# Performance work log

Hardware: AMD Instinct MI355X
Metric: run time of the kernel (lower is better)

Reference implementation:

```python
import jax, jax.numpy as jnp
import numpy as np

B, T, C, H = 8, 2048, 1024, 128  # batch, seq, n_embed, head_size


def setup_inputs() -> dict:
    key = jax.random.key(0)
    ks = jax.random.split(key, 7)
    s = 1.0 / np.sqrt(C)
    return {
        "x": jax.random.normal(ks[0], (B, T, C), dtype=jnp.float32),
        "Wq": jax.random.uniform(ks[1], (C, H), jnp.float32, -s, s),
        "bq": jax.random.uniform(ks[2], (H,), jnp.float32, -s, s),
        "Wk": jax.random.uniform(ks[3], (C, H), jnp.float32, -s, s),
        "bk": jax.random.uniform(ks[4], (H,), jnp.float32, -s, s),
        "Wv": jax.random.uniform(ks[5], (C, H), jnp.float32, -s, s),
        "bv": jax.random.uniform(ks[6], (H,), jnp.float32, -s, s),
    }


def reference(x, Wq, bq, Wk, bk, Wv, bv):
    # Projections: [B, T, H]
    Q = jnp.einsum("btc,ch->bth", x, Wq) + bq
    K = jnp.einsum("btc,ch->bth", x, Wk) + bk
    V = jnp.einsum("btc,ch->bth", x, Wv) + bv
    # Scores scaled by n_embed**-0.5 (faithful to source, which uses C not head_size)
    scale = jnp.asarray(C, x.dtype) ** -0.5
    scores = jnp.einsum("bqh,bkh->bqk", Q, K) * scale  # [B, T, T]
    causal = jnp.tril(jnp.ones((T, T), dtype=bool))
    scores = jnp.where(causal, scores, jnp.asarray(-jnp.inf, x.dtype))
    attn = jax.nn.softmax(scores, axis=-1)
    # dropout p=0.0 (eval) -> identity
    return jnp.einsum("bqk,bkh->bqh", attn, V)
```

## Files before the change

### kernel.cpp

```cpp
#include <hip/hip_runtime.h>
#include <hip/hip_bf16.h>
#include <math.h>

typedef __attribute__((ext_vector_type(4))) float f32x4;
typedef __attribute__((ext_vector_type(8))) short s16x8;
typedef __attribute__((ext_vector_type(4))) short s16x4;

#define NB 8
#define NT 2048
#define NC 1024
#define NH 128
#define QSCALE 0.04508422002778f
#define PIECES 80

__device__ __forceinline__ short f2bf(float f) {
  __hip_bfloat16 h = __float2bfloat16(f);
  union { __hip_bfloat16 h; short s; } u; u.h = h;
  return u.s;
}

__device__ __forceinline__ void glds16(const short* g, short* l) {
  __builtin_amdgcn_global_load_lds(
      (const __attribute__((address_space(1))) unsigned int*)g,
      (__attribute__((address_space(3))) unsigned int*)l, 16, 0, 0);
}

__global__ __launch_bounds__(256)
void wt_kernel(const float* __restrict__ Wq, const float* __restrict__ Wk,
               const float* __restrict__ Wv, short* __restrict__ Wt) {
  __shared__ short T[64 * 72];
  const int tid = threadIdx.x;
  const int k0 = blockIdx.x * 64, n0 = blockIdx.y * 64, proj = blockIdx.z;
  const float* W = (proj == 0) ? Wq : ((proj == 1) ? Wk : Wv);
#pragma unroll
  for (int u = 0; u < 4; u++) {
    int row = u * 16 + (tid >> 4);
    int col4 = (tid & 15) * 4;
    float4 v = *(const float4*)(W + (size_t)(k0 + row) * NH + n0 + col4);
    T[(col4 + 0) * 72 + row] = f2bf(v.x);
    T[(col4 + 1) * 72 + row] = f2bf(v.y);
    T[(col4 + 2) * 72 + row] = f2bf(v.z);
    T[(col4 + 3) * 72 + row] = f2bf(v.w);
  }
  __syncthreads();
#pragma unroll
  for (int u = 0; u < 2; u++) {
    int c = tid + 256 * u;
    int n = c >> 3, c8 = c & 7;
    s16x8 v = *(const s16x8*)(T + n * 72 + c8 * 8);
    *(s16x8*)(Wt + (size_t)proj * (NH * NC) + (size_t)(n0 + n) * NC + k0 + c8 * 8) = v;
  }
}

__global__ __launch_bounds__(256, 3)
void proj_kernel(const float* __restrict__ x, const short* __restrict__ Wt,
                 const float* __restrict__ bq, const float* __restrict__ bk,
                 const float* __restrict__ bv,
                 short* __restrict__ Qb, short* __restrict__ Kb, short* __restrict__ Vtb) {
  __shared__ __align__(16) short smem[2 * 12288];

  const int tid = threadIdx.x;
  const int w = tid >> 6, lane = tid & 63;
  const int lr = lane & 15, lg = lane >> 4;
  const int proj = blockIdx.x;
  const int m0 = blockIdx.y * 64;
  const int msub = (w & 1) * 32, nsub = (w >> 1) * 64;

  const short* Wtp = Wt + (size_t)proj * (NH * NC);
  const int arow = tid >> 2, aq = tid & 3;
  const float* asrc = x + (size_t)(m0 + arow) * NC + aq * 16;

  f32x4 acc[2][4];
#pragma unroll
  for (int i = 0; i < 2; i++)
#pragma unroll
    for (int j = 0; j < 4; j++) acc[i][j] = {0.f, 0.f, 0.f, 0.f};

  float4 pa[2][4];

  auto loadA = [&](int slot, int k0) {
#pragma unroll
    for (int u = 0; u < 4; u++) pa[slot][u] = *(const float4*)(asrc + k0 + u * 4);
  };
  auto writeA = [&](int slot, int buf) {
    short* As = smem + buf * 12288;
#pragma unroll
    for (int h = 0; h < 2; h++) {
      float4 a = pa[slot][2 * h], b2 = pa[slot][2 * h + 1];
      s16x8 v;
      v[0] = f2bf(a.x); v[1] = f2bf(a.y); v[2] = f2bf(a.z); v[3] = f2bf(a.w);
      v[4] = f2bf(b2.x); v[5] = f2bf(b2.y); v[6] = f2bf(b2.z); v[7] = f2bf(b2.w);
      int cc = aq * 2 + h;
      *(s16x8*)(As + arow * 64 + ((cc ^ (arow & 7)) * 8)) = v;
    }
  };
  auto stageB = [&](int buf, int k0) {
    short* Bs = smem + buf * 12288 + 4096;
#pragma unroll
    for (int u = 0; u < 4; u++) {
      int c = u * 256 + w * 64 + lane;
      int n = c >> 3, ch = c & 7;
      glds16(Wtp + (size_t)n * NC + k0 + ((ch ^ (n & 7)) * 8),
             Bs + (u * 256 + w * 64) * 8);
    }
  };
  auto compute = [&](int buf) {
    const short* As = smem + buf * 12288;
    const short* Bs = smem + buf * 12288 + 4096;
#pragma unroll
    for (int kc = 0; kc < 2; kc++) {
      s16x8 af[2], bf[4];
#pragma unroll
      for (int mi = 0; mi < 2; mi++) {
        int row = msub + mi * 16 + lr;
        af[mi] = *(const s16x8*)(As + row * 64 + (((kc * 4 + lg) ^ (row & 7)) * 8));
      }
#pragma unroll
      for (int ni = 0; ni < 4; ni++) {
        int row = nsub + ni * 16 + lr;
        bf[ni] = *(const s16x8*)(Bs + row * 64 + (((kc * 4 + lg) ^ (row & 7)) * 8));
      }
#pragma unroll
      for (int mi = 0; mi < 2; mi++)
#pragma unroll
        for (int ni = 0; ni < 4; ni++)
          acc[mi][ni] = __builtin_amdgcn_mfma_f32_16x16x32_bf16(af[mi], bf[ni], acc[mi][ni], 0, 0, 0);
    }
  };

  loadA(0, 0);
  stageB(0, 0);
  writeA(0, 0);
  __syncthreads();

  for (int s = 0; s < 16; ++s) {
    int buf = s & 1;
    int slot = (s + 1) & 1;
    if (s < 15) { loadA(slot, (s + 1) * 64); stageB(buf ^ 1, (s + 1) * 64); }
    compute(buf);
    if (s < 15) writeA(slot, buf ^ 1);
    __syncthreads();
  }

  const float* bias = (proj == 0) ? bq : ((proj == 1) ? bk : bv);
  const float scl = (proj == 0) ? QSCALE : 1.0f;
  short* Tr = smem;

  if (proj < 2) {
#pragma unroll
    for (int mi = 0; mi < 2; mi++)
#pragma unroll
      for (int ni = 0; ni < 4; ni++) {
        int d = nsub + ni * 16 + lr;
        float bn = bias[d];
#pragma unroll
        for (int r = 0; r < 4; r++) {
          int t = msub + mi * 16 + lg * 4 + r;
          Tr[t * 136 + d] = f2bf((acc[mi][ni][r] + bn) * scl);
        }
      }
    __syncthreads();
    short* dst = (proj == 0) ? Qb : Kb;
#pragma unroll
    for (int i = 0; i < 4; i++) {
      int c = tid + 256 * i;
      int t = c >> 4, cc = c & 15;
      s16x8 v = *(const s16x8*)(Tr + t * 136 + cc * 8);
      *(s16x8*)(dst + (size_t)(m0 + t) * NH + cc * 8) = v;
    }
  } else {
#pragma unroll
    for (int mi = 0; mi < 2; mi++)
#pragma unroll
      for (int ni = 0; ni < 4; ni++) {
        int d = nsub + ni * 16 + lr;
        float bn = bias[d];
        int t0 = msub + mi * 16 + lg * 4;
        s16x4 v;
        v[0] = f2bf(acc[mi][ni][0] + bn);
        v[1] = f2bf(acc[mi][ni][1] + bn);
        v[2] = f2bf(acc[mi][ni][2] + bn);
        v[3] = f2bf(acc[mi][ni][3] + bn);
        *(s16x4*)(Tr + d * 72 + t0) = v;
      }
    __syncthreads();
    int b = m0 >> 11, t0g = m0 & 2047;
#pragma unroll
    for (int i = 0; i < 4; i++) {
      int c = tid + 256 * i;
      int d = c >> 3, cc = c & 7;
      s16x8 v = *(const s16x8*)(Tr + d * 72 + cc * 8);
      *(s16x8*)(Vtb + (size_t)b * (NH * NT) + (size_t)d * NT + t0g + cc * 8) = v;
    }
  }
}

__global__ __launch_bounds__(256, 2)
void attn_partial(const short* __restrict__ Qb, const short* __restrict__ Kb,
                  const short* __restrict__ Vtb, float* __restrict__ out,
                  float* __restrict__ part, float* __restrict__ partml) {
  __shared__ __align__(16) short smem[32768];

  const int tid = threadIdx.x;
  const int w = tid >> 6, lane = tid & 63;
  const int lr = lane & 15, lg = lane >> 4;

  const int batch = blockIdx.x;
  const int r = (PIECES - 1) - blockIdx.y;
  int j = 0, pfx = 0;
  while (pfx + (j >> 3) + 1 <= r) { pfx += (j >> 3) + 1; j++; }
  const int c = r - pfx;
  const int P = (j >> 3) + 1;
  const int q0 = j * 64;
  const int kv_begin = c * 512;
  const int kv_end = min(kv_begin + 512, (j + 1) * 64);
  const int nsteps = (kv_end - kv_begin) >> 6;

  const short* Kp = Kb + (size_t)batch * NT * NH;
  const short* Vp = Vtb + (size_t)batch * NH * NT;
  const int q = q0 + w * 16 + lr;

  const short* Qrow = Qb + (size_t)(batch * NT + q) * NH;
  s16x8 qf[4];
#pragma unroll
  for (int dc = 0; dc < 4; dc++) qf[dc] = *(const s16x8*)(Qrow + dc * 32 + lg * 8);

  f32x4 acc[8];
#pragma unroll
  for (int i = 0; i < 8; i++) acc[i] = {0.f, 0.f, 0.f, 0.f};
  float m_run = -3.0e38f, l_run = 0.f;

  auto stage = [&](int buf, int kv0) {
#pragma unroll
    for (int u = 0; u < 4; u++) {
      int c2 = u * 256 + w * 64 + lane;
      int row = c2 >> 4, ch = c2 & 15;
      int sch = (ch & 8) | ((ch & 7) ^ (row & 7));
      glds16(Kp + (size_t)(kv0 + row) * NH + sch * 8,
             smem + buf * 8192 + (u * 256 + w * 64) * 8);
    }
#pragma unroll
    for (int u = 0; u < 4; u++) {
      int c2 = u * 256 + w * 64 + lane;
      int d = c2 >> 3, ch = c2 & 7;
      int sch = ch ^ (d & 7);
      glds16(Vp + (size_t)d * NT + kv0 + sch * 8,
             smem + 16384 + buf * 8192 + (u * 256 + w * 64) * 8);
    }
  };

  stage(0, kv_begin);
  __syncthreads();

  for (int s = 0; s < nsteps; s++) {
    const int buf = s & 1;
    const int kv0 = kv_begin + s * 64;
    if (s + 1 < nsteps) stage(buf ^ 1, kv0 + 64);

    const short* Kl = smem + buf * 8192;
    const short* Vl = smem + 16384 + buf * 8192;

    f32x4 st[4];
#pragma unroll
    for (int sub = 0; sub < 4; sub++) st[sub] = {0.f, 0.f, 0.f, 0.f};
#pragma unroll
    for (int dc = 0; dc < 4; dc++) {
      int ch = dc * 4 + lg;
      int sch = (ch & 8) | ((ch & 7) ^ (lr & 7));
#pragma unroll
      for (int sub = 0; sub < 4; sub++) {
        s16x8 kf = *(const s16x8*)(Kl + (sub * 16 + lr) * 128 + sch * 8);
        st[sub] = __builtin_amdgcn_mfma_f32_16x16x32_bf16(kf, qf[dc], st[sub], 0, 0, 0);
      }
    }
    if (kv0 + 63 > q0) {
#pragma unroll
      for (int sub = 0; sub < 4; sub++)
#pragma unroll
        for (int rr = 0; rr < 4; rr++)
          if (kv0 + sub * 16 + lg * 4 + rr > q) st[sub][rr] = -3.0e38f;
    }
    float tm = -3.0e38f;
#pragma unroll
    for (int sub = 0; sub < 4; sub++)
#pragma unroll
      for (int rr = 0; rr < 4; rr++) tm = fmaxf(tm, st[sub][rr]);
    tm = fmaxf(tm, __shfl_xor(tm, 16, 64));
    tm = fmaxf(tm, __shfl_xor(tm, 32, 64));
    float m_new = fmaxf(m_run, tm);
    float corr = exp2f(m_run - m_new);
    float psum = 0.f;
    s16x8 pf[2];
#pragma unroll
    for (int sub = 0; sub < 4; sub++)
#pragma unroll
      for (int rr = 0; rr < 4; rr++) {
        float p = exp2f(st[sub][rr] - m_new);
        psum += p;
        pf[sub >> 1][(sub & 1) * 4 + rr] = f2bf(p);
      }
    psum += __shfl_xor(psum, 16, 64);
    psum += __shfl_xor(psum, 32, 64);
    l_run = l_run * corr + psum;
    m_run = m_new;
#pragma unroll
    for (int i = 0; i < 8; i++) acc[i] *= corr;
#pragma unroll
    for (int ks = 0; ks < 2; ks++)
#pragma unroll
      for (int dm = 0; dm < 8; dm++) {
        int d = dm * 16 + lr;
        const short* vb = Vl + d * 64;
        int ch0 = (ks * 4 + (lg >> 1)) ^ (d & 7);
        int ch1 = ch0 ^ 2;
        s16x4 v0 = *(const s16x4*)(vb + ch0 * 8 + (lg & 1) * 4);
        s16x4 v1 = *(const s16x4*)(vb + ch1 * 8 + (lg & 1) * 4);
        s16x8 vf = __builtin_shufflevector(v0, v1, 0, 1, 2, 3, 4, 5, 6, 7);
        acc[dm] = __builtin_amdgcn_mfma_f32_16x16x32_bf16(vf, pf[ks], acc[dm], 0, 0, 0);
      }
    __syncthreads();
  }

  if (P == 1) {
    const float inv = 1.f / l_run;
    float* orow = out + (size_t)(batch * NT + q) * NH;
#pragma unroll
    for (int dm = 0; dm < 8; dm++) {
      f32x4 v = acc[dm] * inv;
      *(f32x4*)(orow + dm * 16 + lg * 4) = v;
    }
  } else {
    float* pb = part + ((size_t)batch * PIECES + r) * 8192;
    int ql = w * 16 + lr;
#pragma unroll
    for (int dm = 0; dm < 8; dm++)
      *(f32x4*)(pb + ql * 128 + dm * 16 + lg * 4) = acc[dm];
    if (lg == 0) {
      float2* ml = (float2*)partml + ((size_t)batch * PIECES + r) * 64;
      ml[ql] = make_float2(m_run, l_run);
    }
  }
}

__global__ __launch_bounds__(256)
void attn_combine(const float* __restrict__ part, const float* __restrict__ partml,
                  float* __restrict__ out) {
  const int batch = blockIdx.x;
  const int j = 8 + blockIdx.y;
  int pfx = 0;
  for (int jj = 0; jj < j; jj++) pfx += (jj >> 3) + 1;
  const int P = (j >> 3) + 1;
  const int tid = threadIdx.x;
  const int ql = tid >> 2, d0 = (tid & 3) * 32;

  const float2* mlb = (const float2*)partml + ((size_t)batch * PIECES + pfx) * 64 + ql;
  float M = -3.0e38f;
  for (int p = 0; p < P; p++) M = fmaxf(M, mlb[p * 64].x);
  float L = 0.f;
  f32x4 o[8];
#pragma unroll
  for (int u = 0; u < 8; u++) o[u] = {0.f, 0.f, 0.f, 0.f};
  for (int p = 0; p < P; p++) {
    float2 ml = mlb[p * 64];
    float wgt = exp2f(ml.x - M);
    L += wgt * ml.y;
    const float* pb = part + ((size_t)batch * PIECES + pfx + p) * 8192 + ql * 128 + d0;
#pragma unroll
    for (int u = 0; u < 8; u++) o[u] += wgt * *(const f32x4*)(pb + u * 4);
  }
  const float inv = 1.f / L;
  float* orow = out + ((size_t)batch * NT + j * 64 + ql) * NH + d0;
#pragma unroll
  for (int u = 0; u < 8; u++) *(f32x4*)(orow + u * 4) = o[u] * inv;
}

extern "C" void kernel_launch(void* const* d_in, const int* in_sizes, int n_in,
                              void* d_out, int out_size, void* d_ws, size_t ws_size,
                              hipStream_t stream) {
  const float* x = (const float*)d_in[0];
  const float* Wq = (const float*)d_in[1];
  const float* bq = (const float*)d_in[2];
  const float* Wk = (const float*)d_in[3];
  const float* bk = (const float*)d_in[4];
  const float* Wv = (const float*)d_in[5];
  const float* bv = (const float*)d_in[6];
  float* out = (float*)d_out;

  char* ws = (char*)d_ws;
  short* Wt = (short*)ws;
  short* Qb = (short*)(ws + 786432);
  short* Kb = (short*)(ws + 786432 + 4194304);
  short* Vtb = (short*)(ws + 786432 + 2 * 4194304);
  float* part = (float*)(ws + 13369344);
  float* partml = (float*)(ws + 13369344 + 20971520);

  wt_kernel<<<dim3(16, 2, 3), dim3(256), 0, stream>>>(Wq, Wk, Wv, Wt);
  proj_kernel<<<dim3(3, 256), dim3(256), 0, stream>>>(x, Wt, bq, bk, bv, Qb, Kb, Vtb);
  attn_partial<<<dim3(8, PIECES), dim3(256), 0, stream>>>(Qb, Kb, Vtb, out, part, partml);
  attn_combine<<<dim3(8, 24), dim3(256), 0, stream>>>(part, partml, out);
}
```

Baseline: 177.1 us.

## Fuse split-KV combine into attention kernel via atomic counter; XCD-aware proj block mapping

Drops the separate combine kernel. The last-finishing split of each query block, found with an atomic counter, merges the partial results inside attn_partial. The projection grid is flattened and remapped so that all three projections of a row tile land on the same XCD, which should improve L2 reuse of x. The change saves one kernel launch and its tail, but adds a memset, threadfences and a serialized combine at the end of some blocks.

```diff
diff --git a/kernel.cpp b/kernel.cpp
--- a/kernel.cpp
+++ b/kernel.cpp
@@ -62,8 +62,13 @@
   const int tid = threadIdx.x;
   const int w = tid >> 6, lane = tid & 63;
   const int lr = lane & 15, lg = lane >> 4;
-  const int proj = blockIdx.x;
-  const int m0 = blockIdx.y * 64;
+
+  const int bid = blockIdx.x;
+  const int xcd = bid & 7;
+  const int idx = bid >> 3;
+  const int proj = idx % 3;
+  const int m0 = (xcd * 32 + idx / 3) * 64;
+
   const int msub = (w & 1) * 32, nsub = (w >> 1) * 64;
 
   const short* Wtp = Wt + (size_t)proj * (NH * NC);
@@ -198,8 +203,10 @@
 __global__ __launch_bounds__(256, 2)
 void attn_partial(const short* __restrict__ Qb, const short* __restrict__ Kb,
                   const short* __restrict__ Vtb, float* __restrict__ out,
-                  float* __restrict__ part, float* __restrict__ partml) {
+                  float* __restrict__ part, float* __restrict__ partml,
+                  int* __restrict__ cnt) {
   __shared__ __align__(16) short smem[32768];
+  __shared__ int s_flag;
 
   const int tid = threadIdx.x;
   const int w = tid >> 6, lane = tid & 63;
@@ -207,9 +214,9 @@
 
   const int batch = blockIdx.x;
   const int r = (PIECES - 1) - blockIdx.y;
-  int j = 0, pfx = 0;
-  while (pfx + (j >> 3) + 1 <= r) { pfx += (j >> 3) + 1; j++; }
-  const int c = r - pfx;
+  int j = 0, pfx0 = 0;
+  while (pfx0 + (j >> 3) + 1 <= r) { pfx0 += (j >> 3) + 1; j++; }
+  const int c = r - pfx0;
   const int P = (j >> 3) + 1;
   const int q0 = j * 64;
   const int kv_begin = c * 512;
@@ -329,49 +336,53 @@
       f32x4 v = acc[dm] * inv;
       *(f32x4*)(orow + dm * 16 + lg * 4) = v;
     }
-  } else {
+    return;
+  }
+
+  {
     float* pb = part + ((size_t)batch * PIECES + r) * 8192;
-    int ql = w * 16 + lr;
+    int ql0 = w * 16 + lr;
 #pragma unroll
     for (int dm = 0; dm < 8; dm++)
-      *(f32x4*)(pb + ql * 128 + dm * 16 + lg * 4) = acc[dm];
+      *(f32x4*)(pb + ql0 * 128 + dm * 16 + lg * 4) = acc[dm];
     if (lg == 0) {
       float2* ml = (float2*)partml + ((size_t)batch * PIECES + r) * 64;
-      ml[ql] = make_float2(m_run, l_run);
-    }
-  }
-}
-
-__global__ __launch_bounds__(256)
-void attn_combine(const float* __restrict__ part, const float* __restrict__ partml,
-                  float* __restrict__ out) {
-  const int batch = blockIdx.x;
-  const int j = 8 + blockIdx.y;
-  int pfx = 0;
-  for (int jj = 0; jj < j; jj++) pfx += (jj >> 3) + 1;
-  const int P = (j >> 3) + 1;
-  const int tid = threadIdx.x;
-  const int ql = tid >> 2, d0 = (tid & 3) * 32;
-
-  const float2* mlb = (const float2*)partml + ((size_t)batch * PIECES + pfx) * 64 + ql;
-  float M = -3.0e38f;
-  for (int p = 0; p < P; p++) M = fmaxf(M, mlb[p * 64].x);
-  float L = 0.f;
-  f32x4 o[8];
-#pragma unroll
-  for (int u = 0; u < 8; u++) o[u] = {0.f, 0.f, 0.f, 0.f};
-  for (int p = 0; p < P; p++) {
-    float2 ml = mlb[p * 64];
-    float wgt = exp2f(ml.x - M);
-    L += wgt * ml.y;
-    const float* pb = part + ((size_t)batch * PIECES + pfx + p) * 8192 + ql * 128 + d0;
-#pragma unroll
-    for (int u = 0; u < 8; u++) o[u] += wgt * *(const f32x4*)(pb + u * 4);
-  }
-  const float inv = 1.f / L;
-  float* orow = out + ((size_t)batch * NT + j * 64 + ql) * NH + d0;
-#pragma unroll
-  for (int u = 0; u < 8; u++) *(f32x4*)(orow + u * 4) = o[u] * inv;
+      ml[ql0] = make_float2(m_run, l_run);
+    }
+  }
+  __threadfence();
+  __syncthreads();
+  if (tid == 0) {
+    int gid = batch * 24 + (j - 8);
+    s_flag = (atomicAdd(&cnt[gid], 1) == P - 1) ? 1 : 0;
+  }
+  __syncthreads();
+  if (!s_flag) return;
+  __threadfence();
+
+  {
+    const int pfx = r - c;
+    const int ql = tid >> 2, d0 = (tid & 3) * 32;
+    const float2* mlb = (const float2*)partml + ((size_t)batch * PIECES + pfx) * 64 + ql;
+    float M = -3.0e38f;
+    for (int p = 0; p < P; p++) M = fmaxf(M, mlb[p * 64].x);
+    float L = 0.f;
+    f32x4 o[8];
+#pragma unroll
+    for (int u = 0; u < 8; u++) o[u] = {0.f, 0.f, 0.f, 0.f};
+    for (int p = 0; p < P; p++) {
+      float2 ml2 = mlb[p * 64];
+      float wgt = exp2f(ml2.x - M);
+      L += wgt * ml2.y;
+      const float* pb2 = part + ((size_t)batch * PIECES + pfx + p) * 8192 + ql * 128 + d0;
+#pragma unroll
+      for (int u = 0; u < 8; u++) o[u] += wgt * *(const f32x4*)(pb2 + u * 4);
+    }
+    const float inv = 1.f / L;
+    float* orow = out + ((size_t)batch * NT + q0 + ql) * NH + d0;
+#pragma unroll
+    for (int u = 0; u < 8; u++) *(f32x4*)(orow + u * 4) = o[u] * inv;
+  }
 }
 
 extern "C" void kernel_launch(void* const* d_in, const int* in_sizes, int n_in,
@@ -393,9 +404,10 @@
   short* Vtb = (short*)(ws + 786432 + 2 * 4194304);
   float* part = (float*)(ws + 13369344);
   float* partml = (float*)(ws + 13369344 + 20971520);
-
+  int* cnt = (int*)(ws + 13369344 + 20971520 + 327680);
+
+  hipMemsetAsync(cnt, 0, 8 * 24 * sizeof(int), stream);
   wt_kernel<<<dim3(16, 2, 3), dim3(256), 0, stream>>>(Wq, Wk, Wv, Wt);
-  proj_kernel<<<dim3(3, 256), dim3(256), 0, stream>>>(x, Wt, bq, bk, bv, Qb, Kb, Vtb);
-  attn_partial<<<dim3(8, PIECES), dim3(256), 0, stream>>>(Qb, Kb, Vtb, out, part, partml);
-  attn_combine<<<dim3(8, 24), dim3(256), 0, stream>>>(part, partml, out);
-}
+  proj_kernel<<<dim3(768), dim3(256), 0, stream>>>(x, Wt, bq, bk, bv, Qb, Kb, Vtb);
+  attn_partial<<<dim3(8, PIECES), dim3(256), 0, stream>>>(Qb, Kb, Vtb, out, part, partml, cnt);
+}
```

Measured after the change: 256.4 us. +44.7%, slower.

## Shrink projection tiles, load A directly into registers, remap blocks by XCD

Applied to the files above, without the earlier changes.

The projection kernel now uses 32-row M tiles instead of 64 and a 1D grid of 1536 blocks. Each block index is decoded so that the three projections of the same rows land on the same XCD, which should improve L2 reuse of x. The A operand (x) is loaded straight from global memory into registers and converted to bf16 in the MFMA fragment layout, so the LDS staging of A is gone and only the weights are staged in LDS. The smaller tiles and LDS use allow 4 blocks per CU, at the cost of less reuse of each B tile per block and uncoalesced per-lane loads of x.

```diff
diff --git a/kernel.cpp b/kernel.cpp
--- a/kernel.cpp
+++ b/kernel.cpp
@@ -52,117 +52,96 @@
   }
 }
 
-__global__ __launch_bounds__(256, 3)
+__global__ __launch_bounds__(256, 4)
 void proj_kernel(const float* __restrict__ x, const short* __restrict__ Wt,
                  const float* __restrict__ bq, const float* __restrict__ bk,
                  const float* __restrict__ bv,
                  short* __restrict__ Qb, short* __restrict__ Kb, short* __restrict__ Vtb) {
-  __shared__ __align__(16) short smem[2 * 12288];
+  __shared__ __align__(16) short Bs[2][8192];
 
   const int tid = threadIdx.x;
   const int w = tid >> 6, lane = tid & 63;
   const int lr = lane & 15, lg = lane >> 4;
-  const int proj = blockIdx.x;
-  const int m0 = blockIdx.y * 64;
-  const int msub = (w & 1) * 32, nsub = (w >> 1) * 64;
+
+  const int bid = blockIdx.x;
+  const int xcd = bid & 7;
+  const int idx = bid >> 3;
+  const int proj = idx % 3;
+  const int m0 = (xcd * 64 + idx / 3) * 32;
+
+  const int msub = (w & 1) * 16, nsub = (w >> 1) * 64;
 
   const short* Wtp = Wt + (size_t)proj * (NH * NC);
-  const int arow = tid >> 2, aq = tid & 3;
-  const float* asrc = x + (size_t)(m0 + arow) * NC + aq * 16;
-
-  f32x4 acc[2][4];
-#pragma unroll
-  for (int i = 0; i < 2; i++)
-#pragma unroll
-    for (int j = 0; j < 4; j++) acc[i][j] = {0.f, 0.f, 0.f, 0.f};
-
-  float4 pa[2][4];
-
-  auto loadA = [&](int slot, int k0) {
-#pragma unroll
-    for (int u = 0; u < 4; u++) pa[slot][u] = *(const float4*)(asrc + k0 + u * 4);
-  };
-  auto writeA = [&](int slot, int buf) {
-    short* As = smem + buf * 12288;
-#pragma unroll
-    for (int h = 0; h < 2; h++) {
-      float4 a = pa[slot][2 * h], b2 = pa[slot][2 * h + 1];
-      s16x8 v;
-      v[0] = f2bf(a.x); v[1] = f2bf(a.y); v[2] = f2bf(a.z); v[3] = f2bf(a.w);
-      v[4] = f2bf(b2.x); v[5] = f2bf(b2.y); v[6] = f2bf(b2.z); v[7] = f2bf(b2.w);
-      int cc = aq * 2 + h;
-      *(s16x8*)(As + arow * 64 + ((cc ^ (arow & 7)) * 8)) = v;
-    }
+  const float* arow = x + (size_t)(m0 + msub + lr) * NC;
+
+  f32x4 acc[4];
+#pragma unroll
+  for (int i = 0; i < 4; i++) acc[i] = {0.f, 0.f, 0.f, 0.f};
+
+  float4 pa[2][2], pn[2][2];
+
+  auto loadA = [&](float4 (&dst)[2][2], int k0) {
+#pragma unroll
+    for (int kc = 0; kc < 2; kc++)
+#pragma unroll
+      for (int h = 0; h < 2; h++)
+        dst[kc][h] = *(const float4*)(arow + k0 + kc * 32 + lg * 8 + h * 4);
   };
   auto stageB = [&](int buf, int k0) {
-    short* Bs = smem + buf * 12288 + 4096;
 #pragma unroll
     for (int u = 0; u < 4; u++) {
       int c = u * 256 + w * 64 + lane;
       int n = c >> 3, ch = c & 7;
       glds16(Wtp + (size_t)n * NC + k0 + ((ch ^ (n & 7)) * 8),
-             Bs + (u * 256 + w * 64) * 8);
-    }
-  };
-  auto compute = [&](int buf) {
-    const short* As = smem + buf * 12288;
-    const short* Bs = smem + buf * 12288 + 4096;
+             &Bs[buf][(u * 256 + w * 64) * 8]);
+    }
+  };
+  auto compute = [&](int buf, float4 (&cur)[2][2]) {
 #pragma unroll
     for (int kc = 0; kc < 2; kc++) {
-      s16x8 af[2], bf[4];
-#pragma unroll
-      for (int mi = 0; mi < 2; mi++) {
-        int row = msub + mi * 16 + lr;
-        af[mi] = *(const s16x8*)(As + row * 64 + (((kc * 4 + lg) ^ (row & 7)) * 8));
-      }
+      float4 a = cur[kc][0], b2 = cur[kc][1];
+      s16x8 af;
+      af[0] = f2bf(a.x); af[1] = f2bf(a.y); af[2] = f2bf(a.z); af[3] = f2bf(a.w);
+      af[4] = f2bf(b2.x); af[5] = f2bf(b2.y); af[6] = f2bf(b2.z); af[7] = f2bf(b2.w);
 #pragma unroll
       for (int ni = 0; ni < 4; ni++) {
         int row = nsub + ni * 16 + lr;
-        bf[ni] = *(const s16x8*)(Bs + row * 64 + (((kc * 4 + lg) ^ (row & 7)) * 8));
-      }
-#pragma unroll
-      for (int mi = 0; mi < 2; mi++)
-#pragma unroll
-        for (int ni = 0; ni < 4; ni++)
-          acc[mi][ni] = __builtin_amdgcn_mfma_f32_16x16x32_bf16(af[mi], bf[ni], acc[mi][ni], 0, 0, 0);
-    }
-  };
-
-  loadA(0, 0);
+        s16x8 bf = *(const s16x8*)(&Bs[buf][row * 64 + (((kc * 4 + lg) ^ (row & 7)) * 8)]);
+        acc[ni] = __builtin_amdgcn_mfma_f32_16x16x32_bf16(af, bf, acc[ni], 0, 0, 0);
+      }
+    }
+  };
+  auto step = [&](int s, float4 (&cur)[2][2], float4 (&nxt)[2][2]) {
+    if (s < 15) { loadA(nxt, (s + 1) * 64); stageB((s & 1) ^ 1, (s + 1) * 64); }
+    compute(s & 1, cur);
+    __syncthreads();
+  };
+
+  loadA(pa, 0);
   stageB(0, 0);
-  writeA(0, 0);
   __syncthreads();
 
-  for (int s = 0; s < 16; ++s) {
-    int buf = s & 1;
-    int slot = (s + 1) & 1;
-    if (s < 15) { loadA(slot, (s + 1) * 64); stageB(buf ^ 1, (s + 1) * 64); }
-    compute(buf);
-    if (s < 15) writeA(slot, buf ^ 1);
-    __syncthreads();
-  }
+  for (int ss = 0; ss < 8; ss++) { step(2 * ss, pa, pn); step(2 * ss + 1, pn, pa); }
 
   const float* bias = (proj == 0) ? bq : ((proj == 1) ? bk : bv);
   const float scl = (proj == 0) ? QSCALE : 1.0f;
-  short* Tr = smem;
+  short* Tr = &Bs[0][0];
 
   if (proj < 2) {
 #pragma unroll
-    for (int mi = 0; mi < 2; mi++)
-#pragma unroll
-      for (int ni = 0; ni < 4; ni++) {
-        int d = nsub + ni * 16 + lr;
-        float bn = bias[d];
-#pragma unroll
-        for (int r = 0; r < 4; r++) {
-          int t = msub + mi * 16 + lg * 4 + r;
-          Tr[t * 136 + d] = f2bf((acc[mi][ni][r] + bn) * scl);
-        }
-      }
+    for (int ni = 0; ni < 4; ni++) {
+      int d = nsub + ni * 16 + lr;
+      float bn = bias[d];
+#pragma unroll
+      for (int r = 0; r < 4; r++) {
+        int t = msub + lg * 4 + r;
+        Tr[t * 136 + d] = f2bf((acc[ni][r] + bn) * scl);
+      }
+    }
     __syncthreads();
     short* dst = (proj == 0) ? Qb : Kb;
 #pragma unroll
-    for (int i = 0; i < 4; i++) {
+    for (int i = 0; i < 2; i++) {
       int c = tid + 256 * i;
       int t = c >> 4, cc = c & 15;
       s16x8 v = *(const s16x8*)(Tr + t * 136 + cc * 8);
@@ -170,26 +149,24 @@
     }
   } else {
 #pragma unroll
-    for (int mi = 0; mi < 2; mi++)
-#pragma unroll
-      for (int ni = 0; ni < 4; ni++) {
-        int d = nsub + ni * 16 + lr;
-        float bn = bias[d];
-        int t0 = msub + mi * 16 + lg * 4;
-        s16x4 v;
-        v[0] = f2bf(acc[mi][ni][0] + bn);
-        v[1] = f2bf(acc[mi][ni][1] + bn);
-        v[2] = f2bf(acc[mi][ni][2] + bn);
-        v[3] = f2bf(acc[mi][ni][3] + bn);
-        *(s16x4*)(Tr + d * 72 + t0) = v;
-      }
+    for (int ni = 0; ni < 4; ni++) {
+      int d = nsub + ni * 16 + lr;
+      float bn = bias[d];
+      int t0 = msub + lg * 4;
+      s16x4 v;
+      v[0] = f2bf(acc[ni][0] + bn);
+      v[1] = f2bf(acc[ni][1] + bn);
+      v[2] = f2bf(acc[ni][2] + bn);
+      v[3] = f2bf(acc[ni][3] + bn);
+      *(s16x4*)(Tr + d * 40 + t0) = v;
+    }
     __syncthreads();
     int b = m0 >> 11, t0g = m0 & 2047;
 #pragma unroll
-    for (int i = 0; i < 4; i++) {
+    for (int i = 0; i < 2; i++) {
       int c = tid + 256 * i;
-      int d = c >> 3, cc = c & 7;
-      s16x8 v = *(const s16x8*)(Tr + d * 72 + cc * 8);
+      int d = c >> 2, cc = c & 3;
+      s16x8 v = *(const s16x8*)(Tr + d * 40 + cc * 8);
       *(s16x8*)(Vtb + (size_t)b * (NH * NT) + (size_t)d * NT + t0g + cc * 8) = v;
     }
   }
@@ -207,9 +184,9 @@
 
   const int batch = blockIdx.x;
   const int r = (PIECES - 1) - blockIdx.y;
-  int j = 0, pfx = 0;
-  while (pfx + (j >> 3) + 1 <= r) { pfx += (j >> 3) + 1; j++; }
-  const int c = r - pfx;
+  int j = 0, pfx0 = 0;
+  while (pfx0 + (j >> 3) + 1 <= r) { pfx0 += (j >> 3) + 1; j++; }
+  const int c = r - pfx0;
   const int P = (j >> 3) + 1;
   const int q0 = j * 64;
   const int kv_begin = c * 512;
@@ -395,7 +372,7 @@
   float* partml = (float*)(ws + 13369344 + 20971520);
 
   wt_kernel<<<dim3(16, 2, 3), dim3(256), 0, stream>>>(Wq, Wk, Wv, Wt);
-  proj_kernel<<<dim3(3, 256), dim3(256), 0, stream>>>(x, Wt, bq, bk, bv, Qb, Kb, Vtb);
+  proj_kernel<<<dim3(1536), dim3(256), 0, stream>>>(x, Wt, bq, bk, bv, Qb, Kb, Vtb);
   attn_partial<<<dim3(8, PIECES), dim3(256), 0, stream>>>(Qb, Kb, Vtb, out, part, partml);
   attn_combine<<<dim3(8, 24), dim3(256), 0, stream>>>(part, partml, out);
 }
```

Result: slower. 205.6 us (+16.0%).
